# Performance work log

Measured on AMD Instinct MI355X. Metric: run time of the kernel, lower is better.

The kernel has to match this reference:

```python
import jax, jax.numpy as jnp
import numpy as np

BN_EPS = 1e-5

def gin_layer(x, src, dst, w1, b1, w2, b2, gamma, beta):
    # GINConv with eps=0: h_i = MLP(x_i + sum_{j->i} x_j)
    agg = jax.ops.segment_sum(x[src], dst, num_segments=x.shape[0])  # [N, D]
    h = x + agg
    h = jnp.maximum(h @ w1 + b1, 0.0) @ w2 + b2
    # BatchNorm (training-mode batch statistics, biased var as in torch)
    mu = jnp.mean(h, axis=0)
    var = jnp.var(h, axis=0)
    h = (h - mu) * jax.lax.rsqrt(var + BN_EPS) * gamma + beta
    return jnp.maximum(h, 0.0)  # ReLU (dropout = identity in eval)

def setup_inputs() -> dict:
    key = jax.random.key(0)
    N, E, G = 20000, 320000, 64
    dims = [128, 128, 256, 512]
    ks = jax.random.split(key, 32)
    inp = {
        "x": jax.random.normal(ks[0], (N, dims[0]), dtype=jnp.float32),
        "edge_index": jax.random.randint(ks[1], (2, E), 0, N, dtype=jnp.int64),
        "batch_idx": jnp.sort(jax.random.randint(ks[2], (N,), 0, G, dtype=jnp.int64)),
    }
    ki = 3
    for li, (di, do) in enumerate(zip(dims[:-1], dims[1:])):
        s = chr(ord('a') + li)
        inp[f"w1{s}"] = jax.random.normal(ks[ki], (di, do), dtype=jnp.float32) * (1.0 / np.sqrt(di)); ki += 1
        inp[f"b1{s}"] = jnp.zeros((do,), dtype=jnp.float32)
        inp[f"w2{s}"] = jax.random.normal(ks[ki], (do, do), dtype=jnp.float32) * (1.0 / np.sqrt(do)); ki += 1
        inp[f"b2{s}"] = jnp.zeros((do,), dtype=jnp.float32)
        inp[f"gn{s}"] = jnp.ones((do,), dtype=jnp.float32)
        inp[f"bn{s}"] = jnp.zeros((do,), dtype=jnp.float32)
    inp["wo"] = jax.random.normal(ks[ki], (dims[-1], 64), dtype=jnp.float32) * (1.0 / np.sqrt(dims[-1]))
    inp["bo"] = jnp.zeros((64,), dtype=jnp.float32)
    return inp

def reference(x, edge_index, batch_idx,
              w1a, b1a, w2a, b2a, gna, bna,
              w1b, b1b, w2b, b2b, gnb, bnb,
              w1c, b1c, w2c, b2c, gnc, bnc,
              wo, bo):
    G = 64
    src, dst = edge_index[0], edge_index[1]
    h = gin_layer(x, src, dst, w1a, b1a, w2a, b2a, gna, bna)
    h = gin_layer(h, src, dst, w1b, b1b, w2b, b2b, gnb, bnb)
    h = gin_layer(h, src, dst, w1c, b1c, w2c, b2c, gnc, bnc)
    # global mean pool over graphs
    sums = jax.ops.segment_sum(h, batch_idx, num_segments=G)  # [G, 512]
    cnts = jax.ops.segment_sum(jnp.ones((h.shape[0],), h.dtype), batch_idx, num_segments=G)
    pooled = sums / jnp.maximum(cnts, 1.0)[:, None]
    # output projection: Linear -> ReLU (dropout identity in eval)
    return jnp.maximum(pooled @ wo + bo, 0.0)
```

## Files before the change

kernel.cpp:

```cpp
#include <hip/hip_runtime.h>

typedef float f32x4 __attribute__((ext_vector_type(4)));
typedef _Float16 f16x2 __attribute__((ext_vector_type(2)));
typedef _Float16 f16x4 __attribute__((ext_vector_type(4)));
typedef _Float16 f16x8 __attribute__((ext_vector_type(8)));

__global__ __launch_bounds__(256) void hist_kernel(const int* __restrict__ dst,
                                                   int* __restrict__ deg, int E) {
  int e = blockIdx.x * 256 + threadIdx.x;
  if (e < E) atomicAdd(&deg[dst[e]], 1);
}

__global__ __launch_bounds__(1024) void scan_kernel(const int* __restrict__ deg,
                                                    int* __restrict__ rowstart,
                                                    int* __restrict__ cursor, int N) {
  __shared__ int sums[1024];
  const int t = threadIdx.x;
  const int CH = (N + 1023) >> 10;
  int local[32];
  int base = t * CH;
  int s = 0;
  for (int i = 0; i < CH; i++) {
    int idx = base + i;
    int v = (idx < N) ? deg[idx] : 0;
    local[i] = s;
    s += v;
  }
  sums[t] = s;
  __syncthreads();
  for (int off = 1; off < 1024; off <<= 1) {
    int add = (t >= off) ? sums[t - off] : 0;
    __syncthreads();
    sums[t] += add;
    __syncthreads();
  }
  int prefix = sums[t] - s;
  for (int i = 0; i < CH; i++) {
    int idx = base + i;
    if (idx < N) {
      int v = prefix + local[i];
      rowstart[idx] = v;
      cursor[idx] = v;
    }
  }
  if (t == 1023) rowstart[N] = sums[1023];
}

__global__ __launch_bounds__(256) void fill_kernel(const int* __restrict__ src,
                                                   const int* __restrict__ dst,
                                                   int* __restrict__ cursor,
                                                   int* __restrict__ nbr, int E) {
  int e = blockIdx.x * 256 + threadIdx.x;
  if (e >= E) return;
  int pos = atomicAdd(&cursor[dst[e]], 1);
  nbr[pos] = src[e];
}

__global__ __launch_bounds__(256) void xprep_kernel(const float4* __restrict__ in,
                                                    f16x4* __restrict__ out, int n4) {
  int i = blockIdx.x * 256 + threadIdx.x;
  if (i >= n4) return;
  float4 v = in[i];
  f16x4 h;
  h[0] = (_Float16)v.x; h[1] = (_Float16)v.y;
  h[2] = (_Float16)v.z; h[3] = (_Float16)v.w;
  out[i] = h;
}

template <int C, bool BNIN>
__global__ __launch_bounds__(256) void gather_agg_kernel(
    const _Float16* __restrict__ x, const int* __restrict__ rowstart,
    const int* __restrict__ nbr, const float* __restrict__ stats,
    _Float16* __restrict__ agg, int N) {
  constexpr int Din = 64 * C;
  const int wave = threadIdx.x >> 6;
  const int lane = threadIdx.x & 63;
  const int node = blockIdx.x * 4 + wave;
  if (node >= N) return;

  float sc[C], sh[C];
  if constexpr (BNIN) {
#pragma unroll
    for (int j = 0; j < C; j++) {
      sc[j] = stats[lane * C + j];
      sh[j] = stats[Din + lane * C + j];
    }
  }

#define LOADROW(dstv, rowidx)                                              \
  {                                                                        \
    const _Float16* _p = x + (size_t)(rowidx)*Din + lane * C;              \
    if constexpr (C == 2) {                                                \
      f16x2 _t = *(const f16x2*)_p;                                        \
      dstv[0] = (float)_t[0]; dstv[1] = (float)_t[1];                      \
    } else {                                                               \
      f16x4 _t = *(const f16x4*)_p;                                        \
      dstv[0] = (float)_t[0]; dstv[1] = (float)_t[1];                      \
      dstv[2] = (float)_t[2]; dstv[3] = (float)_t[3];                      \
    }                                                                      \
  }

  float acc[C];
  {
    float v[C];
    LOADROW(v, node)
#pragma unroll
    for (int j = 0; j < C; j++)
      acc[j] = BNIN ? fmaxf(v[j] * sc[j] + sh[j], 0.f) : v[j];
  }
  const int rs = rowstart[node], re = rowstart[node + 1];
  int e = rs;
  for (; e + 1 < re; e += 2) {
    int s0 = nbr[e], s1 = nbr[e + 1];
    float v0[C], v1[C];
    LOADROW(v0, s0)
    LOADROW(v1, s1)
#pragma unroll
    for (int j = 0; j < C; j++) {
      acc[j] += BNIN ? fmaxf(v0[j] * sc[j] + sh[j], 0.f) : v0[j];
      acc[j] += BNIN ? fmaxf(v1[j] * sc[j] + sh[j], 0.f) : v1[j];
    }
  }
  if (e < re) {
    int s0 = nbr[e];
    float v0[C];
    LOADROW(v0, s0)
#pragma unroll
    for (int j = 0; j < C; j++)
      acc[j] += BNIN ? fmaxf(v0[j] * sc[j] + sh[j], 0.f) : v0[j];
  }
#undef LOADROW

  _Float16* o = agg + (size_t)node * Din + lane * C;
  if constexpr (C == 2) {
    f16x2 r; r[0] = (_Float16)acc[0]; r[1] = (_Float16)acc[1];
    *(f16x2*)o = r;
  } else {
    f16x4 r;
    r[0] = (_Float16)acc[0]; r[1] = (_Float16)acc[1];
    r[2] = (_Float16)acc[2]; r[3] = (_Float16)acc[3];
    *(f16x4*)o = r;
  }
}

struct WSeg {
  const float* W;
  _Float16* TH;
  int K, N, total;
};
struct WAll { WSeg s[6]; };

__global__ __launch_bounds__(256) void wprep_all_kernel(WAll a) {
  WSeg sg = a.s[blockIdx.y];
  int idx = blockIdx.x * 256 + threadIdx.x;
  if (idx >= sg.total) return;
  int k = idx / sg.N, n = idx - k * sg.N;
  sg.TH[(size_t)n * sg.K + k] = (_Float16)sg.W[idx];
}

template <int RT>
__global__ __launch_bounds__(256, 8) void gemm_mfma_kernel(
    const _Float16* __restrict__ A, const _Float16* __restrict__ BT,
    const float* __restrict__ bias, _Float16* __restrict__ Ch,
    int M, int K, int N, int mblocks, int cbShift,
    int doRelu, float* __restrict__ stats) {
  constexpr int NF = RT / 16;
  constexpr int NP = RT / 32;
  __shared__ _Float16 Ah[2 * NF * 512];
  const int bid = blockIdx.x;
  const int xcd = bid & 7;
  const int q = bid >> 3;
  const int r = ((q >> cbShift) << 3) + xcd;
  const int cb = q & ((1 << cbShift) - 1);
  if (r >= mblocks) return;

  const int tid = threadIdx.x;
  const int lane = tid & 63;
  const int w = tid >> 6;
  const int rowBase = r * RT;
  const int colBase = cb * 128 + w * 32;

  f32x4 acc[NF][2] = {};

  const int c0 = colBase + (lane & 15);
  const int kfrag = (lane >> 4) * 8;

  int srow, slane, sfrag0, kk0;
  if constexpr (RT == 64) {
    srow = tid >> 2;
    const int schunk = tid & 3;
    slane = (srow & 15) | (schunk << 4);
    sfrag0 = srow >> 4;
    kk0 = schunk * 8;
  } else {
    srow = tid >> 3;
    const int c8 = tid & 7;
    const int lc = c8 & 3, ks = c8 >> 2;
    slane = (srow & 15) | (lc << 4);
    sfrag0 = ks * NF + (srow >> 4);
    kk0 = lc * 8 + ks * 32;
  }
  const size_t arowOff = (size_t)(rowBase + srow) * K;
  const bool srowOk = (rowBase + srow) < M;

  for (int k0 = 0; k0 < K; k0 += 64) {
#pragma unroll
    for (int i = 0; i < NP; i++) {
      int kk = k0 + kk0 + (RT == 64 ? i * 32 : 0);
      f16x8 h8 = {};
      if (srowOk) h8 = *(const f16x8*)(A + arowOff + kk);
      int frag = (RT == 64 ? i * NF + sfrag0 : sfrag0);
      *(f16x8*)(Ah + frag * 512 + slane * 8) = h8;
    }
    __syncthreads();
#pragma unroll
    for (int ks = 0; ks < 2; ks++) {
      int kidx = k0 + ks * 32 + kfrag;
      f16x8 bh0 = *(const f16x8*)(BT + (size_t)c0 * K + kidx);
      f16x8 bh1 = *(const f16x8*)(BT + (size_t)(c0 + 16) * K + kidx);
#pragma unroll
      for (int fi = 0; fi < NF; fi++) {
        int frag = ks * NF + fi;
        f16x8 ah = *(const f16x8*)(Ah + frag * 512 + lane * 8);
        acc[fi][0] = __builtin_amdgcn_mfma_f32_16x16x32_f16(ah, bh0, acc[fi][0], 0, 0, 0);
        acc[fi][1] = __builtin_amdgcn_mfma_f32_16x16x32_f16(ah, bh1, acc[fi][1], 0, 0, 0);
      }
    }
    __syncthreads();
  }

  const float bias0 = bias[c0], bias1 = bias[c0 + 16];
  float s1[2] = {0.f, 0.f}, s2[2] = {0.f, 0.f};
  const int rbase = rowBase + (lane >> 4) * 4;
#pragma unroll
  for (int fi = 0; fi < NF; fi++) {
#pragma unroll
    for (int j = 0; j < 4; j++) {
      int row = rbase + fi * 16 + j;
      float v0 = acc[fi][0][j] + bias0;
      float v1 = acc[fi][1][j] + bias1;
      if (doRelu) { v0 = fmaxf(v0, 0.f); v1 = fmaxf(v1, 0.f); }
      if (row < M) {
        Ch[(size_t)row * N + c0] = (_Float16)v0;
        Ch[(size_t)row * N + c0 + 16] = (_Float16)v1;
        s1[0] += v0; s2[0] += v0 * v0;
        s1[1] += v1; s2[1] += v1 * v1;
      }
    }
  }
  if (stats) {
#pragma unroll
    for (int off = 16; off < 64; off <<= 1) {
      s1[0] += __shfl_xor(s1[0], off);
      s2[0] += __shfl_xor(s2[0], off);
      s1[1] += __shfl_xor(s1[1], off);
      s2[1] += __shfl_xor(s2[1], off);
    }
    if (lane < 16) {
      atomicAdd(&stats[c0], s1[0]);
      atomicAdd(&stats[N + c0], s2[0]);
      atomicAdd(&stats[c0 + 16], s1[1]);
      atomicAdd(&stats[N + c0 + 16], s2[1]);
    }
  }
}

__global__ __launch_bounds__(256) void bn_prep_kernel(float* __restrict__ stats,
                                                      const float* __restrict__ gamma,
                                                      const float* __restrict__ beta,
                                                      int D, float invN) {
  int c = blockIdx.x * 256 + threadIdx.x;
  if (c >= D) return;
  float mean = stats[c] * invN;
  float var = stats[D + c] * invN - mean * mean;
  float sc = rsqrtf(var + 1e-5f) * gamma[c];
  stats[c] = sc;
  stats[D + c] = beta[c] - mean * sc;
}

__global__ __launch_bounds__(256) void bn_pool_kernel(
    const _Float16* __restrict__ h, const float* __restrict__ stats,
    const int* __restrict__ batch, float* __restrict__ pooled, int N) {
  const int g = blockIdx.x >> 3;
  const int s = blockIdx.x & 7;
  __shared__ int s_lo, s_hi;
  if (threadIdx.x == 0) {
    int lo = 0, hi = N;
    while (lo < hi) { int m = (lo + hi) >> 1; if (batch[m] < g) lo = m + 1; else hi = m; }
    s_lo = lo;
    lo = 0; hi = N;
    while (lo < hi) { int m = (lo + hi) >> 1; if (batch[m] < g + 1) lo = m + 1; else hi = m; }
    s_hi = lo;
  }
  __syncthreads();
  const int lo = s_lo, hi = s_hi, len = hi - lo;
  if (len == 0) return;
  const int per = (len + 7) >> 3;
  const int rs = lo + s * per;
  const int re = min(rs + per, hi);
  if (rs >= re) return;
  const int t = threadIdx.x;
  float2 sc = *(const float2*)(stats + 2 * t);
  float2 sh = *(const float2*)(stats + 512 + 2 * t);
  float ax = 0.f, ay = 0.f;
  for (int r = rs; r < re; r++) {
    f16x2 v = *(const f16x2*)(h + (size_t)r * 512 + 2 * t);
    ax += fmaxf((float)v[0] * sc.x + sh.x, 0.f);
    ay += fmaxf((float)v[1] * sc.y + sh.y, 0.f);
  }
  float inv = 1.f / (float)len;
  atomicAdd(&pooled[g * 512 + 2 * t], ax * inv);
  atomicAdd(&pooled[g * 512 + 2 * t + 1], ay * inv);
}

__global__ __launch_bounds__(64) void out_kernel(const float* __restrict__ pooled,
                                                 const float* __restrict__ wo,
                                                 const float* __restrict__ bo,
                                                 float* __restrict__ out) {
  int g = blockIdx.x, o = threadIdx.x;
  float acc = bo[o];
  for (int c = 0; c < 512; c++) acc += pooled[g * 512 + c] * wo[c * 64 + o];
  out[g * 64 + o] = fmaxf(acc, 0.f);
}

extern "C" void kernel_launch(void* const* d_in, const int* in_sizes, int n_in,
                              void* d_out, int out_size, void* d_ws, size_t ws_size,
                              hipStream_t stream) {
  const float* x0 = (const float*)d_in[0];
  const int* ei = (const int*)d_in[1];
  const int* batch = (const int*)d_in[2];
  const int N = in_sizes[0] / 128;
  const int E = in_sizes[1] / 2;
  const int* src = ei;
  const int* dst = ei + E;
  const float* W[3][6];
  for (int li = 0; li < 3; li++)
    for (int k = 0; k < 6; k++) W[li][k] = (const float*)d_in[3 + li * 6 + k];
  const float* wo = (const float*)d_in[21];
  const float* bo = (const float*)d_in[22];
  float* out = (float*)d_out;

  float* stats3 = (float*)d_ws;
  float* pooled = stats3 + 3 * 1024;
  int* deg = (int*)(pooled + 64 * 512);
  int* rowstart = deg + N;
  int* cursor = rowstart + N + 1;
  int* nbr = cursor + N;
  uintptr_t wp = (uintptr_t)(nbr + E);
  wp = (wp + 15) & ~(uintptr_t)15;
  _Float16* aggh = (_Float16*)wp;
  _Float16* h1h = aggh + (size_t)N * 256;
  _Float16* h2h = h1h + (size_t)N * 512;
  _Float16* x0h = h2h + (size_t)N * 512;
  _Float16* wbuf = x0h + (size_t)N * 128;

  const int dins[3] = {128, 128, 256};
  const int douts[3] = {128, 256, 512};

  _Float16* WT[3][2];
  {
    _Float16* p = wbuf;
    for (int li = 0; li < 3; li++) {
      WT[li][0] = p; p += (size_t)dins[li] * douts[li];
      WT[li][1] = p; p += (size_t)douts[li] * douts[li];
    }
  }
  {
    WAll wa;
    int maxTotal = 0;
    for (int li = 0; li < 3; li++) {
      int e1 = dins[li] * douts[li];
      int e2 = douts[li] * douts[li];
      wa.s[li * 2 + 0] = WSeg{W[li][0], WT[li][0], dins[li], douts[li], e1};
      wa.s[li * 2 + 1] = WSeg{W[li][2], WT[li][1], douts[li], douts[li], e2};
      maxTotal = max(maxTotal, max(e1, e2));
    }
    dim3 g((maxTotal + 255) / 256, 6);
    wprep_all_kernel<<<g, 256, 0, stream>>>(wa);
  }

  {
    int n4 = N * 32;
    xprep_kernel<<<(n4 + 255) / 256, 256, 0, stream>>>((const float4*)x0, (f16x4*)x0h, n4);
  }

  hipMemsetAsync(deg, 0, (size_t)N * sizeof(int), stream);
  hist_kernel<<<(E + 255) / 256, 256, 0, stream>>>(dst, deg, E);
  scan_kernel<<<1, 1024, 0, stream>>>(deg, rowstart, cursor, N);
  fill_kernel<<<(E + 255) / 256, 256, 0, stream>>>(src, dst, cursor, nbr, E);

  hipMemsetAsync(stats3, 0, (3 * 1024 + 64 * 512) * sizeof(float), stream);

  const int mb64 = (N + 63) / 64;
  const int mb64_8 = ((mb64 + 7) / 8) * 8;
  const int mb32 = (N + 31) / 32;
  const int mb32_8 = ((mb32 + 7) / 8) * 8;
  const int gblocks = (N + 3) / 4;

  for (int li = 0; li < 3; li++) {
    int Din = dins[li], Dout = douts[li];
    float* stats = stats3 + li * 1024;
    if (li == 0)
      gather_agg_kernel<2, false><<<gblocks, 256, 0, stream>>>(x0h, rowstart, nbr, nullptr, aggh, N);
    else if (li == 1)
      gather_agg_kernel<2, true><<<gblocks, 256, 0, stream>>>(h2h, rowstart, nbr, stats3 + 0 * 1024, aggh, N);
    else
      gather_agg_kernel<4, true><<<gblocks, 256, 0, stream>>>(h2h, rowstart, nbr, stats3 + 1 * 1024, aggh, N);

    if (Dout == 128) {
      gemm_mfma_kernel<32><<<mb32_8, 256, 0, stream>>>(aggh, WT[li][0], W[li][1], h1h,
                                                       N, Din, Dout, mb32, 0, 1, nullptr);
      gemm_mfma_kernel<32><<<mb32_8, 256, 0, stream>>>(h1h, WT[li][1], W[li][3], h2h,
                                                       N, Dout, Dout, mb32, 0, 0, stats);
    } else {
      int cbShift = (Dout == 256) ? 1 : 2;
      int nblocks = mb64_8 << cbShift;
      gemm_mfma_kernel<64><<<nblocks, 256, 0, stream>>>(aggh, WT[li][0], W[li][1], h1h,
                                                        N, Din, Dout, mb64, cbShift, 1, nullptr);
      gemm_mfma_kernel<64><<<nblocks, 256, 0, stream>>>(h1h, WT[li][1], W[li][3], h2h,
                                                        N, Dout, Dout, mb64, cbShift, 0, stats);
    }
    bn_prep_kernel<<<(Dout + 255) / 256, 256, 0, stream>>>(stats, W[li][4], W[li][5], Dout, 1.0f / N);
    if (li == 2) {
      bn_pool_kernel<<<64 * 8, 256, 0, stream>>>(h2h, stats, batch, pooled, N);
    }
  }
  out_kernel<<<64, 64, 0, stream>>>(pooled, wo, bo, out);
}
```

Measured before the change: 310.2 us.

## Fuse both MLP GEMMs per layer into one kernel keeping hidden tile in LDS

Replaces the two separate GEMM launches per GIN layer with one mlp_kernel. It computes Linear→ReLU into shared memory for a 32-row tile, then the second Linear plus bias and the BatchNorm statistic accumulation, so the hidden activation never goes through global memory. BN scale and shift are now computed inline in the consumers (gather and pool), which removes the bn_prep launches. The cost is large LDS use for the wide layer (32×256 + 32×512 halves), which lowers occupancy. Each block also handles all output columns with fewer blocks, and B weights are reloaded from global memory per block.

```diff
diff --git a/kernel.cpp b/kernel.cpp
--- a/kernel.cpp
+++ b/kernel.cpp
@@ -71,7 +71,8 @@
 __global__ __launch_bounds__(256) void gather_agg_kernel(
     const _Float16* __restrict__ x, const int* __restrict__ rowstart,
     const int* __restrict__ nbr, const float* __restrict__ stats,
-    _Float16* __restrict__ agg, int N) {
+    const float* __restrict__ gamma, const float* __restrict__ beta,
+    _Float16* __restrict__ agg, int N, float invN) {
   constexpr int Din = 64 * C;
   const int wave = threadIdx.x >> 6;
   const int lane = threadIdx.x & 63;
@@ -82,8 +83,11 @@
   if constexpr (BNIN) {
 #pragma unroll
     for (int j = 0; j < C; j++) {
-      sc[j] = stats[lane * C + j];
-      sh[j] = stats[Din + lane * C + j];
+      int c = lane * C + j;
+      float mean = stats[c] * invN;
+      float var = stats[Din + c] * invN - mean * mean;
+      sc[j] = rsqrtf(var + 1e-5f) * gamma[c];
+      sh[j] = beta[c] - mean * sc[j];
     }
   }
 
@@ -158,129 +162,138 @@
   sg.TH[(size_t)n * sg.K + k] = (_Float16)sg.W[idx];
 }
 
-template <int RT>
-__global__ __launch_bounds__(256, 8) void gemm_mfma_kernel(
-    const _Float16* __restrict__ A, const _Float16* __restrict__ BT,
-    const float* __restrict__ bias, _Float16* __restrict__ Ch,
-    int M, int K, int N, int mblocks, int cbShift,
-    int doRelu, float* __restrict__ stats) {
-  constexpr int NF = RT / 16;
-  constexpr int NP = RT / 32;
-  __shared__ _Float16 Ah[2 * NF * 512];
-  const int bid = blockIdx.x;
-  const int xcd = bid & 7;
-  const int q = bid >> 3;
-  const int r = ((q >> cbShift) << 3) + xcd;
-  const int cb = q & ((1 << cbShift) - 1);
-  if (r >= mblocks) return;
+template <int DIN, int DOUT>
+__global__ __launch_bounds__(256) void mlp_kernel(
+    const _Float16* __restrict__ A, const _Float16* __restrict__ B1T,
+    const float* __restrict__ bias1, const _Float16* __restrict__ B2T,
+    const float* __restrict__ bias2, _Float16* __restrict__ H2,
+    int M, float* __restrict__ stats) {
+  constexpr int CW = DOUT / 4;
+  constexpr int NCF = CW / 16;
+  constexpr int KS1 = DIN / 32;
+  constexpr int KS2 = DOUT / 32;
+  __shared__ _Float16 Atile[32 * DIN];
+  __shared__ _Float16 H1[32 * DOUT];
 
   const int tid = threadIdx.x;
   const int lane = tid & 63;
   const int w = tid >> 6;
-  const int rowBase = r * RT;
-  const int colBase = cb * 128 + w * 32;
-
-  f32x4 acc[NF][2] = {};
-
+  const int rowBase = blockIdx.x * 32;
+  const int colBase = w * CW;
   const int c0 = colBase + (lane & 15);
-  const int kfrag = (lane >> 4) * 8;
-
-  int srow, slane, sfrag0, kk0;
-  if constexpr (RT == 64) {
-    srow = tid >> 2;
-    const int schunk = tid & 3;
-    slane = (srow & 15) | (schunk << 4);
-    sfrag0 = srow >> 4;
-    kk0 = schunk * 8;
-  } else {
-    srow = tid >> 3;
+  const int kf = (lane >> 4) * 8;
+
+  {
+    const int srow = tid >> 3;
     const int c8 = tid & 7;
-    const int lc = c8 & 3, ks = c8 >> 2;
-    slane = (srow & 15) | (lc << 4);
-    sfrag0 = ks * NF + (srow >> 4);
-    kk0 = lc * 8 + ks * 32;
-  }
-  const size_t arowOff = (size_t)(rowBase + srow) * K;
-  const bool srowOk = (rowBase + srow) < M;
-
-  for (int k0 = 0; k0 < K; k0 += 64) {
-#pragma unroll
-    for (int i = 0; i < NP; i++) {
-      int kk = k0 + kk0 + (RT == 64 ? i * 32 : 0);
+    const size_t aoff = (size_t)(rowBase + srow) * DIN;
+    const bool ok = (rowBase + srow) < M;
+#pragma unroll
+    for (int i = 0; i < DIN / 64; i++) {
+      int k = c8 * 8 + i * 64;
       f16x8 h8 = {};
-      if (srowOk) h8 = *(const f16x8*)(A + arowOff + kk);
-      int frag = (RT == 64 ? i * NF + sfrag0 : sfrag0);
-      *(f16x8*)(Ah + frag * 512 + slane * 8) = h8;
-    }
-    __syncthreads();
-#pragma unroll
-    for (int ks = 0; ks < 2; ks++) {
-      int kidx = k0 + ks * 32 + kfrag;
-      f16x8 bh0 = *(const f16x8*)(BT + (size_t)c0 * K + kidx);
-      f16x8 bh1 = *(const f16x8*)(BT + (size_t)(c0 + 16) * K + kidx);
-#pragma unroll
-      for (int fi = 0; fi < NF; fi++) {
-        int frag = ks * NF + fi;
-        f16x8 ah = *(const f16x8*)(Ah + frag * 512 + lane * 8);
-        acc[fi][0] = __builtin_amdgcn_mfma_f32_16x16x32_f16(ah, bh0, acc[fi][0], 0, 0, 0);
-        acc[fi][1] = __builtin_amdgcn_mfma_f32_16x16x32_f16(ah, bh1, acc[fi][1], 0, 0, 0);
-      }
-    }
-    __syncthreads();
-  }
-
-  const float bias0 = bias[c0], bias1 = bias[c0 + 16];
-  float s1[2] = {0.f, 0.f}, s2[2] = {0.f, 0.f};
-  const int rbase = rowBase + (lane >> 4) * 4;
-#pragma unroll
-  for (int fi = 0; fi < NF; fi++) {
-#pragma unroll
-    for (int j = 0; j < 4; j++) {
-      int row = rbase + fi * 16 + j;
-      float v0 = acc[fi][0][j] + bias0;
-      float v1 = acc[fi][1][j] + bias1;
-      if (doRelu) { v0 = fmaxf(v0, 0.f); v1 = fmaxf(v1, 0.f); }
-      if (row < M) {
-        Ch[(size_t)row * N + c0] = (_Float16)v0;
-        Ch[(size_t)row * N + c0 + 16] = (_Float16)v1;
-        s1[0] += v0; s2[0] += v0 * v0;
-        s1[1] += v1; s2[1] += v1 * v1;
-      }
-    }
-  }
-  if (stats) {
-#pragma unroll
-    for (int off = 16; off < 64; off <<= 1) {
-      s1[0] += __shfl_xor(s1[0], off);
-      s2[0] += __shfl_xor(s2[0], off);
-      s1[1] += __shfl_xor(s1[1], off);
-      s2[1] += __shfl_xor(s2[1], off);
+      if (ok) h8 = *(const f16x8*)(A + aoff + k);
+      int frag = (k >> 5) * 2 + (srow >> 4);
+      int slot = (srow & 15) | (((k >> 3) & 3) << 4);
+      *(f16x8*)(Atile + frag * 512 + slot * 8) = h8;
+    }
+  }
+  __syncthreads();
+
+  {
+    f32x4 acc[2][NCF] = {};
+#pragma unroll
+    for (int ks = 0; ks < KS1; ks++) {
+      f16x8 b1[NCF];
+#pragma unroll
+      for (int cf = 0; cf < NCF; cf++)
+        b1[cf] = *(const f16x8*)(B1T + (size_t)(c0 + cf * 16) * DIN + ks * 32 + kf);
+#pragma unroll
+      for (int fi = 0; fi < 2; fi++) {
+        f16x8 a = *(const f16x8*)(Atile + (ks * 2 + fi) * 512 + lane * 8);
+#pragma unroll
+        for (int cf = 0; cf < NCF; cf++)
+          acc[fi][cf] = __builtin_amdgcn_mfma_f32_16x16x32_f16(b1[cf], a, acc[fi][cf], 0, 0, 0);
+      }
+    }
+#pragma unroll
+    for (int cf = 0; cf < NCF; cf++) {
+      const int c = colBase + cf * 16 + (lane >> 4) * 4;
+      float4 b4 = *(const float4*)(bias1 + c);
+#pragma unroll
+      for (int fi = 0; fi < 2; fi++) {
+        f16x4 hv;
+#pragma unroll
+        for (int j = 0; j < 4; j++)
+          hv[j] = (_Float16)fmaxf(acc[fi][cf][j] + ((const float*)&b4)[j], 0.f);
+        int frag = (c >> 5) * 2 + fi;
+        int slot = (lane & 15) | (((c >> 3) & 3) << 4);
+        *(f16x4*)(H1 + frag * 512 + slot * 8 + (c & 7)) = hv;
+      }
+    }
+  }
+  __syncthreads();
+
+  {
+    f32x4 acc[2][NCF] = {};
+#pragma unroll
+    for (int ks = 0; ks < KS2; ks++) {
+      f16x8 b2[NCF];
+#pragma unroll
+      for (int cf = 0; cf < NCF; cf++)
+        b2[cf] = *(const f16x8*)(B2T + (size_t)(c0 + cf * 16) * DOUT + ks * 32 + kf);
+#pragma unroll
+      for (int fi = 0; fi < 2; fi++) {
+        f16x8 a = *(const f16x8*)(H1 + (ks * 2 + fi) * 512 + lane * 8);
+#pragma unroll
+        for (int cf = 0; cf < NCF; cf++)
+          acc[fi][cf] = __builtin_amdgcn_mfma_f32_16x16x32_f16(a, b2[cf], acc[fi][cf], 0, 0, 0);
+      }
+    }
+    float bs[NCF], s1[NCF], s2[NCF];
+#pragma unroll
+    for (int cf = 0; cf < NCF; cf++) {
+      bs[cf] = bias2[c0 + cf * 16];
+      s1[cf] = 0.f; s2[cf] = 0.f;
+    }
+    const int rbase = rowBase + (lane >> 4) * 4;
+#pragma unroll
+    for (int fi = 0; fi < 2; fi++) {
+#pragma unroll
+      for (int j = 0; j < 4; j++) {
+        int row = rbase + fi * 16 + j;
+        if (row < M) {
+#pragma unroll
+          for (int cf = 0; cf < NCF; cf++) {
+            float v = acc[fi][cf][j] + bs[cf];
+            H2[(size_t)row * DOUT + c0 + cf * 16] = (_Float16)v;
+            s1[cf] += v; s2[cf] += v * v;
+          }
+        }
+      }
+    }
+#pragma unroll
+    for (int cf = 0; cf < NCF; cf++) {
+#pragma unroll
+      for (int off = 16; off < 64; off <<= 1) {
+        s1[cf] += __shfl_xor(s1[cf], off);
+        s2[cf] += __shfl_xor(s2[cf], off);
+      }
     }
     if (lane < 16) {
-      atomicAdd(&stats[c0], s1[0]);
-      atomicAdd(&stats[N + c0], s2[0]);
-      atomicAdd(&stats[c0 + 16], s1[1]);
-      atomicAdd(&stats[N + c0 + 16], s2[1]);
-    }
-  }
-}
-
-__global__ __launch_bounds__(256) void bn_prep_kernel(float* __restrict__ stats,
-                                                      const float* __restrict__ gamma,
-                                                      const float* __restrict__ beta,
-                                                      int D, float invN) {
-  int c = blockIdx.x * 256 + threadIdx.x;
-  if (c >= D) return;
-  float mean = stats[c] * invN;
-  float var = stats[D + c] * invN - mean * mean;
-  float sc = rsqrtf(var + 1e-5f) * gamma[c];
-  stats[c] = sc;
-  stats[D + c] = beta[c] - mean * sc;
+#pragma unroll
+      for (int cf = 0; cf < NCF; cf++) {
+        atomicAdd(&stats[c0 + cf * 16], s1[cf]);
+        atomicAdd(&stats[DOUT + c0 + cf * 16], s2[cf]);
+      }
+    }
+  }
 }
 
 __global__ __launch_bounds__(256) void bn_pool_kernel(
     const _Float16* __restrict__ h, const float* __restrict__ stats,
-    const int* __restrict__ batch, float* __restrict__ pooled, int N) {
+    const float* __restrict__ gamma, const float* __restrict__ beta,
+    const int* __restrict__ batch, float* __restrict__ pooled, int N, float invN) {
   const int g = blockIdx.x >> 3;
   const int s = blockIdx.x & 7;
   __shared__ int s_lo, s_hi;
@@ -300,13 +313,20 @@
   const int re = min(rs + per, hi);
   if (rs >= re) return;
   const int t = threadIdx.x;
-  float2 sc = *(const float2*)(stats + 2 * t);
-  float2 sh = *(const float2*)(stats + 512 + 2 * t);
+  float scv[2], shv[2];
+#pragma unroll
+  for (int j = 0; j < 2; j++) {
+    int c = 2 * t + j;
+    float mean = stats[c] * invN;
+    float var = stats[512 + c] * invN - mean * mean;
+    scv[j] = rsqrtf(var + 1e-5f) * gamma[c];
+    shv[j] = beta[c] - mean * scv[j];
+  }
   float ax = 0.f, ay = 0.f;
   for (int r = rs; r < re; r++) {
     f16x2 v = *(const f16x2*)(h + (size_t)r * 512 + 2 * t);
-    ax += fmaxf((float)v[0] * sc.x + sh.x, 0.f);
-    ay += fmaxf((float)v[1] * sc.y + sh.y, 0.f);
+    ax += fmaxf((float)v[0] * scv[0] + shv[0], 0.f);
+    ay += fmaxf((float)v[1] * scv[1] + shv[1], 0.f);
   }
   float inv = 1.f / (float)len;
   atomicAdd(&pooled[g * 512 + 2 * t], ax * inv);
@@ -349,8 +369,7 @@
   uintptr_t wp = (uintptr_t)(nbr + E);
   wp = (wp + 15) & ~(uintptr_t)15;
   _Float16* aggh = (_Float16*)wp;
-  _Float16* h1h = aggh + (size_t)N * 256;
-  _Float16* h2h = h1h + (size_t)N * 512;
+  _Float16* h2h = aggh + (size_t)N * 256;
   _Float16* x0h = h2h + (size_t)N * 512;
   _Float16* wbuf = x0h + (size_t)N * 128;
 
@@ -391,39 +410,26 @@
 
   hipMemsetAsync(stats3, 0, (3 * 1024 + 64 * 512) * sizeof(float), stream);
 
-  const int mb64 = (N + 63) / 64;
-  const int mb64_8 = ((mb64 + 7) / 8) * 8;
   const int mb32 = (N + 31) / 32;
-  const int mb32_8 = ((mb32 + 7) / 8) * 8;
   const int gblocks = (N + 3) / 4;
-
-  for (int li = 0; li < 3; li++) {
-    int Din = dins[li], Dout = douts[li];
-    float* stats = stats3 + li * 1024;
-    if (li == 0)
-      gather_agg_kernel<2, false><<<gblocks, 256, 0, stream>>>(x0h, rowstart, nbr, nullptr, aggh, N);
-    else if (li == 1)
-      gather_agg_kernel<2, true><<<gblocks, 256, 0, stream>>>(h2h, rowstart, nbr, stats3 + 0 * 1024, aggh, N);
-    else
-      gather_agg_kernel<4, true><<<gblocks, 256, 0, stream>>>(h2h, rowstart, nbr, stats3 + 1 * 1024, aggh, N);
-
-    if (Dout == 128) {
-      gemm_mfma_kernel<32><<<mb32_8, 256, 0, stream>>>(aggh, WT[li][0], W[li][1], h1h,
-                                                       N, Din, Dout, mb32, 0, 1, nullptr);
-      gemm_mfma_kernel<32><<<mb32_8, 256, 0, stream>>>(h1h, WT[li][1], W[li][3], h2h,
-                                                       N, Dout, Dout, mb32, 0, 0, stats);
-    } else {
-      int cbShift = (Dout == 256) ? 1 : 2;
-      int nblocks = mb64_8 << cbShift;
-      gemm_mfma_kernel<64><<<nblocks, 256, 0, stream>>>(aggh, WT[li][0], W[li][1], h1h,
-                                                        N, Din, Dout, mb64, cbShift, 1, nullptr);
-      gemm_mfma_kernel<64><<<nblocks, 256, 0, stream>>>(h1h, WT[li][1], W[li][3], h2h,
-                                                        N, Dout, Dout, mb64, cbShift, 0, stats);
-    }
-    bn_prep_kernel<<<(Dout + 255) / 256, 256, 0, stream>>>(stats, W[li][4], W[li][5], Dout, 1.0f / N);
-    if (li == 2) {
-      bn_pool_kernel<<<64 * 8, 256, 0, stream>>>(h2h, stats, batch, pooled, N);
-    }
-  }
+  const float invN = 1.0f / N;
+
+  gather_agg_kernel<2, false><<<gblocks, 256, 0, stream>>>(
+      x0h, rowstart, nbr, nullptr, nullptr, nullptr, aggh, N, invN);
+  mlp_kernel<128, 128><<<mb32, 256, 0, stream>>>(
+      aggh, WT[0][0], W[0][1], WT[0][1], W[0][3], h2h, N, stats3 + 0 * 1024);
+
+  gather_agg_kernel<2, true><<<gblocks, 256, 0, stream>>>(
+      h2h, rowstart, nbr, stats3 + 0 * 1024, W[0][4], W[0][5], aggh, N, invN);
+  mlp_kernel<128, 256><<<mb32, 256, 0, stream>>>(
+      aggh, WT[1][0], W[1][1], WT[1][1], W[1][3], h2h, N, stats3 + 1 * 1024);
+
+  gather_agg_kernel<4, true><<<gblocks, 256, 0, stream>>>(
+      h2h, rowstart, nbr, stats3 + 1 * 1024, W[1][4], W[1][5], aggh, N, invN);
+  mlp_kernel<256, 512><<<mb32, 256, 0, stream>>>(
+      aggh, WT[2][0], W[2][1], WT[2][1], W[2][3], h2h, N, stats3 + 2 * 1024);
+
+  bn_pool_kernel<<<64 * 8, 256, 0, stream>>>(
+      h2h, stats3 + 2 * 1024, W[2][4], W[2][5], batch, pooled, N, invN);
   out_kernel<<<64, 64, 0, stream>>>(pooled, wo, bo, out);
 }
```

Measured after the change: 325.9 us. 1.05x slower.
